# Performance work log

Measured on AMD Instinct MI355X. Metric: run time of the kernel, lower is better.

The kernel has to match this reference:

```python
import jax, jax.numpy as jnp
import numpy as np
from jax import lax

BS, C, H, W = 256, 256, 16, 16
NUM_CLASSES = 2
EPS = 1e-12  # F.normalize eps


def _l2_normalize(x):
    # F.normalize(x, dim=1, p=2): x / max(||x||_2, eps) along channel dim
    n = jnp.sqrt(jnp.sum(x * x, axis=1, keepdims=True))
    return x / jnp.maximum(n, EPS)


def _correlation(f1, f2):
    # original: (f1[:, :, None, :, :] * f2.reshape(bs,c,-1)[:, :, :, None, None]).sum(1)
    # -> [bs, h*w, h, w]; expressed as a batched contraction over channels.
    f1n = _l2_normalize(f1)                      # [bs, c, h, w]
    f2n = _l2_normalize(f2).reshape(f2.shape[0], f2.shape[1], -1)  # [bs, c, hw]
    return jnp.einsum('bcxy,bck->bkxy', f1n, f2n)


def _conv3x3(x, w, b):
    y = lax.conv_general_dilated(x, w, (1, 1), 'SAME',
                                 dimension_numbers=('NCHW', 'OIHW', 'NCHW'))
    return y + b[None, :, None, None]


def _psroi_diag(feat, num_classes, h, w):
    # full-image box, pooled==spatial, group_size==h -> each bin is one pixel:
    # out[n, c, ph, pw] = feat[n, (c*h + ph)*w + pw, ph, pw]
    bs = feat.shape[0]
    f = feat.reshape(bs, num_classes, h, w, h, w)
    f = jnp.diagonal(f, axis1=2, axis2=4)   # [bs, nc, w, w, h] (ph diag -> last)
    f = jnp.diagonal(f, axis1=2, axis2=3)   # [bs, nc, h, w]? -> [bs, nc, h_diag, w_diag]
    # after two diagonals axes are [bs, nc, ph, pw]
    return f


def setup_inputs() -> dict:
    key = jax.random.key(0)
    ks = jax.random.split(key, 5)
    std1 = float(np.sqrt(2.0 / (3 * 3 * 1024)))
    std2 = float(np.sqrt(2.0 / (3 * 3 * 512)))
    stdc = float(np.sqrt(2.0 / (1 * 1 * NUM_CLASSES * H * W)))
    return {
        'feature_1': jax.random.normal(ks[0], (BS, C, H, W), jnp.float32),
        'feature_2': jax.random.normal(ks[1], (BS, C, H, W), jnp.float32),
        'conv1_w': jax.random.normal(ks[2], (1024, 2 * (C + H * W), 3, 3), jnp.float32) * std1,
        'conv1_b': jnp.zeros((1024,), jnp.float32),
        'conv2_w': jax.random.normal(ks[3], (512, 1024, 3, 3), jnp.float32) * std2,
        'conv2_b': jnp.zeros((512,), jnp.float32),
        'conv_cls_w': jax.random.normal(ks[4], (NUM_CLASSES * H * W, 512, 1, 1), jnp.float32) * stdc,
    }


def reference(feature_1, feature_2, conv1_w, conv1_b, conv2_w, conv2_b, conv_cls_w):
    f1 = jax.nn.relu(feature_1)
    f2 = jax.nn.relu(feature_2)
    corr1 = _correlation(f1, f2)   # [bs, hw, h, w]
    corr2 = _correlation(f2, f1)
    feat = jnp.concatenate((f1, corr1, f2, corr2), axis=1)  # [bs, 2*(c+hw), h, w]
    feat = jax.nn.relu(_conv3x3(feat, conv1_w, conv1_b))
    feat = jax.nn.relu(_conv3x3(feat, conv2_w, conv2_b))
    feat = jnp.einsum('bchw,oc->bohw', feat, conv_cls_w[:, :, 0, 0])  # 1x1 conv, no bias
    feat = jax.nn.relu(feat)
    cls_base = _psroi_diag(feat, NUM_CLASSES, H, W)      # [bs, nc, h, w]
    cls_score = jnp.mean(cls_base, axis=(2, 3))          # AvgPool2d(h, w)
    cls_prob = jax.nn.softmax(cls_score, axis=1)
    # eval-mode return of the original module
    return (cls_prob, corr1, corr2)
```

## Files before the change

kernel.cpp:

```cpp
#include <hip/hip_runtime.h>


typedef __attribute__((ext_vector_type(8))) __bf16 bf16x8;
typedef __attribute__((ext_vector_type(4))) float f32x4;
typedef unsigned short u16;

template <bool B> struct BC { static constexpr bool value = B; };

__device__ __forceinline__ u16 f2bf(float f) {
  union { float f; unsigned u; } v; v.f = f;
  unsigned u = v.u;
  u += 0x7fffu + ((u >> 16) & 1u);
  return (u16)(u >> 16);
}
__device__ __forceinline__ float bf2f(u16 h) {
  union { unsigned u; float f; } v; v.u = ((unsigned)h) << 16;
  return v.f;
}
__device__ __forceinline__ void gl2lds16(const void* g, void* l) {
  __builtin_amdgcn_global_load_lds(
      (__attribute__((address_space(1))) void*)(void*)g,
      (__attribute__((address_space(3))) void*)l, 16, 0, 0);
}

__global__ __launch_bounds__(256) void k_norm(const float* __restrict__ f1,
                                              const float* __restrict__ f2,
                                              u16* __restrict__ featT,
                                              float* __restrict__ s1,
                                              float* __restrict__ s2) {
  int bx = blockIdx.x;
  int b = bx >> 2;
  int p0 = (bx & 3) << 6;
  int t = threadIdx.x;
  int p = p0 + (t & 63);
  int cg = t >> 6;
  int sp3 = ((p >> 1) & 3) << 3;
  const float* F1 = f1 + ((size_t)b << 16);
  const float* F2 = f2 + ((size_t)b << 16);
  u16* FT = featT + (((size_t)(b << 8) + p) << 10);
  float ss1 = 0.f, ss2 = 0.f;
  for (int i = 0; i < 64; ++i) {
    int c = (cg << 6) + i;
    float v1 = F1[(c << 8) + p]; v1 = v1 > 0.f ? v1 : 0.f;
    float v2 = F2[(c << 8) + p]; v2 = v2 > 0.f ? v2 : 0.f;
    ss1 += v1 * v1; ss2 += v2 * v2;
    FT[c ^ sp3] = f2bf(v1);
    FT[512 + (c ^ sp3)] = f2bf(v2);
  }
  __shared__ float l1[256], l2[256];
  l1[t] = ss1; l2[t] = ss2;
  __syncthreads();
  if (t < 64) {
    float a = l1[t] + l1[t + 64] + l1[t + 128] + l1[t + 192];
    float c2 = l2[t] + l2[t + 64] + l2[t + 128] + l2[t + 192];
    int pp = (b << 8) + p0 + t;
    s1[pp] = 1.f / fmaxf(sqrtf(a), 1e-12f);
    s2[pp] = 1.f / fmaxf(sqrtf(c2), 1e-12f);
  }
}

__global__ __launch_bounds__(256) void k_wconv(const float* __restrict__ w,
                                               u16* __restrict__ wb, int O, int C) {
  int o = blockIdx.x;
  int t = threadIdx.x;
  int sp3 = ((o >> 1) & 3) << 3;
  const float* src = w + (size_t)o * C * 9;
  for (int c = t; c < C; c += 256) {
    const float* s = src + c * 9;
    float v[9];
#pragma unroll
    for (int i = 0; i < 9; ++i) v[i] = s[i];
#pragma unroll
    for (int tap = 0; tap < 9; ++tap)
      wb[(size_t)tap * O * C + (size_t)o * C + (c ^ sp3)] = f2bf(v[tap]);
  }
}

__global__ __launch_bounds__(256) void k_corr(u16* featT,
                                              const float* __restrict__ s1,
                                              const float* __restrict__ s2,
                                              float* __restrict__ out) {
  __shared__ alignas(16) u16 Alds[128 * 32];
  __shared__ alignas(16) u16 Blds[128 * 32];
  __shared__ float tb[4][16][66];
  int bx = blockIdx.x;
  int b = bx >> 2;
  int p1b = ((bx >> 1) & 1) << 7;
  int p2b = (bx & 1) << 7;
  int t = threadIdx.x, l = t & 63, w = t >> 6;
  int wm = w >> 1, wn = w & 1, lr = l & 15, lq = l >> 4;
  int srow = (w << 4) + (l >> 2);
  int sq = (l & 3) << 3;
  int rsz = ((lq ^ ((lr >> 1) & 3)) << 3);
  const size_t bbase = (size_t)b << 18;

  f32x4 acc[4][4];
#pragma unroll
  for (int i = 0; i < 4; ++i)
#pragma unroll
    for (int j = 0; j < 4; ++j) acc[i][j] = (f32x4){0.f, 0.f, 0.f, 0.f};

#pragma unroll 1
  for (int kc = 0; kc < 8; ++kc) {
    int c0 = kc << 5;
    const u16* sA = featT + bbase + ((size_t)(p1b + srow) << 10) + (c0 + sq);
    gl2lds16(sA, Alds + ((w << 4) << 5));
    gl2lds16(sA + (64 << 10), Alds + ((64 + (w << 4)) << 5));
    const u16* sB = featT + bbase + ((size_t)(p2b + srow) << 10) + (512 + c0 + sq);
    gl2lds16(sB, Blds + ((w << 4) << 5));
    gl2lds16(sB + (64 << 10), Blds + ((64 + (w << 4)) << 5));
    __syncthreads();
    bf16x8 af[4], bfr[4];
#pragma unroll
    for (int mf = 0; mf < 4; ++mf)
      af[mf] = *(const bf16x8*)(Alds + (((wm << 6) + (mf << 4) + lr) << 5) + rsz);
#pragma unroll
    for (int nf = 0; nf < 4; ++nf)
      bfr[nf] = *(const bf16x8*)(Blds + (((wn << 6) + (nf << 4) + lr) << 5) + rsz);
#pragma unroll
    for (int mf = 0; mf < 4; ++mf)
#pragma unroll
      for (int nf = 0; nf < 4; ++nf)
        acc[mf][nf] = __builtin_amdgcn_mfma_f32_16x16x32_bf16(af[mf], bfr[nf], acc[mf][nf], 0, 0, 0);
    __syncthreads();
  }

  float sc2[4]; int p2g[4];
#pragma unroll
  for (int nf = 0; nf < 4; ++nf) {
    int p2 = p2b + (wn << 6) + (nf << 4) + lr;
    p2g[nf] = p2;
    sc2[nf] = s2[(b << 8) + p2];
  }
  float* corr1 = out + 512;
  float* corr2 = out + 512 + 16777216;
#pragma unroll
  for (int mf = 0; mf < 4; ++mf) {
    float gv[4][4];
#pragma unroll
    for (int r = 0; r < 4; ++r) {
      int p1 = p1b + (wm << 6) + (mf << 4) + (lq << 2) + r;
      float s1v = s1[(b << 8) + p1];
#pragma unroll
      for (int nf = 0; nf < 4; ++nf) gv[nf][r] = acc[mf][nf][r] * s1v * sc2[nf];
    }
#pragma unroll
    for (int r = 0; r < 4; ++r) {
      int p1 = p1b + (wm << 6) + (mf << 4) + (lq << 2) + r;
      int s1p3 = ((p1 >> 1) & 3) << 3;
#pragma unroll
      for (int nf = 0; nf < 4; ++nf) {
        corr2[((size_t)b << 16) + ((size_t)p1 << 8) + p2g[nf]] = gv[nf][r];
        featT[bbase + ((size_t)p1 << 10) + 256 + (p2g[nf] ^ s1p3)] = f2bf(gv[nf][r]);
      }
    }
#pragma unroll
    for (int r = 0; r < 4; ++r)
#pragma unroll
      for (int nf = 0; nf < 4; ++nf)
        tb[w][(lq << 2) + r][(nf << 4) + lr] = gv[nf][r];
#pragma unroll
    for (int j = 0; j < 16; ++j) {
      float v = tb[w][lr][(j << 2) + lq];
      int p2 = p2b + (wn << 6) + (j << 2) + lq;
      int s2p3 = ((p2 >> 1) & 3) << 3;
      int p1 = p1b + (wm << 6) + (mf << 4) + lr;
      corr1[((size_t)b << 16) + ((size_t)p2 << 8) + p1] = v;
      featT[bbase + ((size_t)p2 << 10) + 768 + (p1 ^ s2p3)] = f2bf(v);
    }
  }
}

template <int O, int OTB>
__global__ __launch_bounds__(512, 4) void k_conv(const u16* __restrict__ X,
                                                 const u16* __restrict__ Wb,
                                                 const float* __restrict__ bias,
                                                 u16* __restrict__ Out) {
  __shared__ alignas(16) u16 Xlds[2][260 * 32];
  __shared__ alignas(16) u16 Wlds[3][128 * 32];
  int bx = blockIdx.x;
  int otile = bx & ((1 << OTB) - 1);
  int b = bx >> OTB;
  int t = threadIdx.x, l = t & 63, w = t >> 6;
  int wm = w & 3, wn = w >> 2;
  int lr = l & 15, lq = l >> 4;
  int o0 = otile << 7;
  int srl = l >> 2;
  int sq = (l & 3) << 3;
  const size_t xbase = (size_t)b << 18;

  const u16* wsrc = Wb + (((size_t)(o0 + (w << 4) + srl)) << 10) + sq;
  const u16* xsrc0 = X + xbase + (((size_t)((w << 4) + srl)) << 10) + sq;
  const u16* xsrc1 = xsrc0 + ((size_t)128 << 10);

  u16* wdst0 = &Wlds[0][(w << 4) << 5];
  u16* wdst1 = &Wlds[1][(w << 4) << 5];
  u16* wdst2 = &Wlds[2][(w << 4) << 5];
  u16* xdA0 = &Xlds[0][(w << 4) << 5];
  u16* xdA1 = &Xlds[0][(128 + (w << 4)) << 5];
  u16* xdB0 = &Xlds[1][(w << 4) << 5];
  u16* xdB1 = &Xlds[1][(128 + (w << 4)) << 5];

  int rszw = ((lq ^ ((lr >> 1) & 3)) << 3);
  const u16* bwb0 = &Wlds[0][(((wn << 6) + lr) << 5) + rszw];
  const u16* bwb1 = &Wlds[1][(((wn << 6) + lr) << 5) + rszw];
  const u16* bwb2 = &Wlds[2][(((wn << 6) + lr) << 5) + rszw];

  int pb[4];
#pragma unroll
  for (int mf = 0; mf < 4; ++mf)
    pb[mf] = (((wm << 6) + (mf << 4) + lr) << 5);
  int xsz[3];
#pragma unroll
  for (int d = 0; d < 3; ++d)
    xsz[d] = ((lq ^ (((lr + d - 1) >> 1) & 3)) << 3);
  const int zoff = (256 << 5) + (lq << 3);

  f32x4 acc[4][4];
#pragma unroll
  for (int i = 0; i < 4; ++i)
#pragma unroll
    for (int j = 0; j < 4; ++j) acc[i][j] = (f32x4){0.f, 0.f, 0.f, 0.f};

  if (t < 32) ((unsigned*)&Xlds[t >> 4][256 << 5])[t & 15] = 0u;

  gl2lds16(xsrc0, xdA0);
  gl2lds16(xsrc1, xdA1);
  gl2lds16(wsrc, wdst0);
  gl2lds16(wsrc + ((size_t)O << 10), wdst1);
  __syncthreads();

  auto kcbody = [&](auto oddc, int kc) {
    constexpr bool ODD = decltype(oddc)::value;
    const u16* xb = ODD ? &Xlds[1][0] : &Xlds[0][0];
#pragma unroll
    for (int tap = 0; tap < 9; ++tap) {
      __builtin_amdgcn_sched_barrier(0);
      int ntap = (tap + 2) % 9;
      int nkc = kc + (tap >= 7 ? 1 : 0);
      u16* wd = ((tap + 2) % 3 == 0) ? wdst0 : (((tap + 2) % 3 == 1) ? wdst1 : wdst2);
      gl2lds16(wsrc + (size_t)ntap * ((size_t)O << 10) + (nkc << 5), wd);
      if (tap == 0) {
        if (ODD) { gl2lds16(xsrc0 + ((kc + 1) << 5), xdA0); gl2lds16(xsrc1 + ((kc + 1) << 5), xdA1); }
        else     { gl2lds16(xsrc0 + ((kc + 1) << 5), xdB0); gl2lds16(xsrc1 + ((kc + 1) << 5), xdB1); }
      }
      const u16* bwb = (tap % 3 == 0) ? bwb0 : ((tap % 3 == 1) ? bwb1 : bwb2);
      bf16x8 bwf[4];
#pragma unroll
      for (int nf = 0; nf < 4; ++nf) bwf[nf] = *(const bf16x8*)(bwb + (nf << 9));
      const int dr = tap / 3 - 1, dc = tap % 3 - 1;
      const int dpo = (((dr << 4) + dc) << 5) + xsz[dc + 1];
      bf16x8 axf[4];
#pragma unroll
      for (int mf = 0; mf < 4; ++mf) {
        int rr = (wm << 2) + mf + dr;
        bool v = ((unsigned)rr < 16u) & ((unsigned)(lr + dc) < 16u);
        int off = v ? (pb[mf] + dpo) : zoff;
        axf[mf] = *(const bf16x8*)(xb + off);
      }
#pragma unroll
      for (int mf = 0; mf < 4; ++mf)
#pragma unroll
        for (int nf = 0; nf < 4; ++nf)
          acc[mf][nf] = __builtin_amdgcn_mfma_f32_16x16x32_bf16(axf[mf], bwf[nf], acc[mf][nf], 0, 0, 0);
      if (tap == 0 || tap == 1) asm volatile("s_waitcnt vmcnt(3)" ::: "memory");
      else                      asm volatile("s_waitcnt vmcnt(1)" ::: "memory");
      __builtin_amdgcn_s_barrier();
    }
  };

#pragma unroll 1
  for (int kc2 = 0; kc2 < 16; ++kc2) {
    kcbody(BC<false>{}, 2 * kc2);
    kcbody(BC<true>{}, 2 * kc2 + 1);
  }

  __syncthreads();
  float bv[4];
#pragma unroll
  for (int nf = 0; nf < 4; ++nf) bv[nf] = bias[o0 + (wn << 6) + (nf << 4) + lr];
  u16* scr = ((u16*)Xlds) + w * 1152;
  int rr2 = l >> 2;
  int kq = l & 3;
#pragma unroll
  for (int mf = 0; mf < 4; ++mf) {
#pragma unroll
    for (int r = 0; r < 4; ++r) {
      int rr = (lq << 2) + r;
#pragma unroll
      for (int nf = 0; nf < 4; ++nf) {
        float vv = acc[mf][nf][r] + bv[nf];
        scr[rr * 72 + (nf << 4) + lr] = f2bf(vv > 0.f ? vv : 0.f);
      }
    }
    asm volatile("s_waitcnt lgkmcnt(0)" ::: "memory");
    __builtin_amdgcn_sched_barrier(0);
    int p = (wm << 6) + (mf << 4) + rr2;
    int sp = (p >> 1) & 3;
    size_t rbase = (size_t)((b << 8) + p) * O + (size_t)(o0 + (wn << 6));
#pragma unroll
    for (int j = 0; j < 2; ++j) {
      int k = (j << 2) | kq;
      int kl = (j << 2) | (kq ^ sp);
      uint4 v = *(const uint4*)(scr + rr2 * 72 + (kl << 3));
      *(uint4*)(Out + rbase + (k << 3)) = v;
    }
    asm volatile("s_waitcnt lgkmcnt(0)" ::: "memory");
    __builtin_amdgcn_sched_barrier(0);
  }
}

__global__ __launch_bounds__(256) void k_cls(const u16* __restrict__ X2,
                                             const float* __restrict__ Wc,
                                             float* __restrict__ out) {
  int b = blockIdx.x, p = threadIdx.x;
  int s = (p >> 1) & 3;
  const uint4* xv = (const uint4*)(X2 + (((size_t)(b << 8) + p) << 9));
  const float4* w0 = (const float4*)(Wc + ((size_t)p << 9));
  const float4* w1 = (const float4*)(Wc + ((size_t)(256 + p) << 9));
  float a0 = 0.f, a1 = 0.f;
#pragma unroll 4
  for (int i = 0; i < 64; ++i) {
    int ii = (i & ~3) | ((i & 3) ^ s);
    uint4 u = xv[ii];
    float x0 = bf2f((u16)(u.x & 0xffffu)), x1 = bf2f((u16)(u.x >> 16));
    float x2 = bf2f((u16)(u.y & 0xffffu)), x3 = bf2f((u16)(u.y >> 16));
    float x4 = bf2f((u16)(u.z & 0xffffu)), x5 = bf2f((u16)(u.z >> 16));
    float x6 = bf2f((u16)(u.w & 0xffffu)), x7 = bf2f((u16)(u.w >> 16));
    float4 wa = w0[i * 2], wb = w0[i * 2 + 1];
    a0 += x0 * wa.x + x1 * wa.y + x2 * wa.z + x3 * wa.w +
          x4 * wb.x + x5 * wb.y + x6 * wb.z + x7 * wb.w;
    float4 wc4 = w1[i * 2], wd = w1[i * 2 + 1];
    a1 += x0 * wc4.x + x1 * wc4.y + x2 * wc4.z + x3 * wc4.w +
          x4 * wd.x + x5 * wd.y + x6 * wd.z + x7 * wd.w;
  }
  a0 = fmaxf(a0, 0.f);
  a1 = fmaxf(a1, 0.f);
  __shared__ float r0[256], r1[256];
  r0[p] = a0; r1[p] = a1;
  for (int sdx = 128; sdx > 0; sdx >>= 1) {
    __syncthreads();
    if (p < sdx) { r0[p] += r0[p + sdx]; r1[p] += r1[p + sdx]; }
  }
  __syncthreads();
  if (p == 0) {
    float s0 = r0[0] * (1.f / 256.f), s1v = r1[0] * (1.f / 256.f);
    float m = fmaxf(s0, s1v);
    float e0 = expf(s0 - m), e1 = expf(s1v - m);
    float inv = 1.f / (e0 + e1);
    out[(b << 1) + 0] = e0 * inv;
    out[(b << 1) + 1] = e1 * inv;
  }
}

extern "C" void kernel_launch(void* const* d_in, const int* in_sizes, int n_in,
                              void* d_out, int out_size, void* d_ws, size_t ws_size,
                              hipStream_t stream) {
  const float* f1 = (const float*)d_in[0];
  const float* f2 = (const float*)d_in[1];
  const float* w1 = (const float*)d_in[2];
  const float* b1 = (const float*)d_in[3];
  const float* w2 = (const float*)d_in[4];
  const float* b2 = (const float*)d_in[5];
  const float* wc = (const float*)d_in[6];
  float* out = (float*)d_out;
  char* ws = (char*)d_ws;

  u16* featT = (u16*)(ws + 0);
  u16* out1T = (u16*)(ws + 134217728);
  u16* W1b   = (u16*)(ws + 268435456);
  u16* W2b   = (u16*)(ws + 287309824);
  float* s1  = (float*)(ws + 296747008);
  float* s2  = (float*)(ws + 297009152);
  u16* out2T = (u16*)(ws + 0);

  k_norm<<<1024, 256, 0, stream>>>(f1, f2, featT, s1, s2);
  k_wconv<<<1024, 256, 0, stream>>>(w1, W1b, 1024, 1024);
  k_wconv<<<512, 256, 0, stream>>>(w2, W2b, 512, 1024);
  k_corr<<<1024, 256, 0, stream>>>(featT, s1, s2, out);
  k_conv<1024, 3><<<2048, 512, 0, stream>>>(featT, W1b, b1, out1T);
  k_conv<512, 2><<<1024, 512, 0, stream>>>(out1T, W2b, b2, out2T);
  k_cls<<<256, 256, 0, stream>>>(out2T, wc, out);
}
```

Measured before the change: 1.902 ms.

## Deepen conv weight prefetch to four LDS buffers and raise MFMA priority

The conv kernel's weight staging grows from three to four rotating LDS buffers, so weight tiles are prefetched three taps ahead instead of two. The k-chunk loop is unrolled by four to keep the buffer rotation compile-time, and the vmcnt waits are relaxed to match. s_setprio is raised around the MFMA block so compute waves are favoured over load issue. The cls kernel now reads the X2 rows in linear order and applies the swizzle to the weight index instead; this uses more LDS per block and enlarges code size, which may affect occupancy.

```diff
diff --git a/kernel.cpp b/kernel.cpp
--- a/kernel.cpp
+++ b/kernel.cpp
@@ -5,7 +5,7 @@
 typedef __attribute__((ext_vector_type(4))) float f32x4;
 typedef unsigned short u16;
 
-template <bool B> struct BC { static constexpr bool value = B; };
+template <int I> struct IC { static constexpr int value = I; };
 
 __device__ __forceinline__ u16 f2bf(float f) {
   union { float f; unsigned u; } v; v.f = f;
@@ -177,7 +177,7 @@
                                                  const float* __restrict__ bias,
                                                  u16* __restrict__ Out) {
   __shared__ alignas(16) u16 Xlds[2][260 * 32];
-  __shared__ alignas(16) u16 Wlds[3][128 * 32];
+  __shared__ alignas(16) u16 Wlds[4][128 * 32];
   int bx = blockIdx.x;
   int otile = bx & ((1 << OTB) - 1);
   int b = bx >> OTB;
@@ -196,6 +196,7 @@
   u16* wdst0 = &Wlds[0][(w << 4) << 5];
   u16* wdst1 = &Wlds[1][(w << 4) << 5];
   u16* wdst2 = &Wlds[2][(w << 4) << 5];
+  u16* wdst3 = &Wlds[3][(w << 4) << 5];
   u16* xdA0 = &Xlds[0][(w << 4) << 5];
   u16* xdA1 = &Xlds[0][(128 + (w << 4)) << 5];
   u16* xdB0 = &Xlds[1][(w << 4) << 5];
@@ -205,6 +206,7 @@
   const u16* bwb0 = &Wlds[0][(((wn << 6) + lr) << 5) + rszw];
   const u16* bwb1 = &Wlds[1][(((wn << 6) + lr) << 5) + rszw];
   const u16* bwb2 = &Wlds[2][(((wn << 6) + lr) << 5) + rszw];
+  const u16* bwb3 = &Wlds[3][(((wn << 6) + lr) << 5) + rszw];
 
   int pb[4];
 #pragma unroll
@@ -228,23 +230,32 @@
   gl2lds16(xsrc1, xdA1);
   gl2lds16(wsrc, wdst0);
   gl2lds16(wsrc + ((size_t)O << 10), wdst1);
-  __syncthreads();
-
-  auto kcbody = [&](auto oddc, int kc) {
-    constexpr bool ODD = decltype(oddc)::value;
-    const u16* xb = ODD ? &Xlds[1][0] : &Xlds[0][0];
+  gl2lds16(wsrc + 2 * ((size_t)O << 10), wdst2);
+  asm volatile("s_waitcnt vmcnt(2) lgkmcnt(0)" ::: "memory");
+  __builtin_amdgcn_s_barrier();
+
+  auto kcbody = [&](auto km4c, int kc) {
+    constexpr int KM4 = decltype(km4c)::value;
+    const u16* xb = (KM4 & 1) ? &Xlds[1][0] : &Xlds[0][0];
 #pragma unroll
     for (int tap = 0; tap < 9; ++tap) {
       __builtin_amdgcn_sched_barrier(0);
-      int ntap = (tap + 2) % 9;
-      int nkc = kc + (tap >= 7 ? 1 : 0);
-      u16* wd = ((tap + 2) % 3 == 0) ? wdst0 : (((tap + 2) % 3 == 1) ? wdst1 : wdst2);
-      gl2lds16(wsrc + (size_t)ntap * ((size_t)O << 10) + (nkc << 5), wd);
+      {
+        int ntap = (tap + 3 > 8) ? (tap - 6) : (tap + 3);
+        int nkc = (tap >= 6) ? (kc + 1) : kc;
+        constexpr int WB = (KM4 + 3) & 3;
+        u16* wd = (((WB + tap) & 3) == 0) ? wdst0
+                : ((((WB + tap) & 3) == 1) ? wdst1
+                : ((((WB + tap) & 3) == 2) ? wdst2 : wdst3));
+        gl2lds16(wsrc + (size_t)ntap * ((size_t)O << 10) + (nkc << 5), wd);
+      }
       if (tap == 0) {
-        if (ODD) { gl2lds16(xsrc0 + ((kc + 1) << 5), xdA0); gl2lds16(xsrc1 + ((kc + 1) << 5), xdA1); }
-        else     { gl2lds16(xsrc0 + ((kc + 1) << 5), xdB0); gl2lds16(xsrc1 + ((kc + 1) << 5), xdB1); }
-      }
-      const u16* bwb = (tap % 3 == 0) ? bwb0 : ((tap % 3 == 1) ? bwb1 : bwb2);
+        if (KM4 & 1) { gl2lds16(xsrc0 + ((kc + 1) << 5), xdA0); gl2lds16(xsrc1 + ((kc + 1) << 5), xdA1); }
+        else         { gl2lds16(xsrc0 + ((kc + 1) << 5), xdB0); gl2lds16(xsrc1 + ((kc + 1) << 5), xdB1); }
+      }
+      const u16* bwb = (((KM4 + tap) & 3) == 0) ? bwb0
+                     : ((((KM4 + tap) & 3) == 1) ? bwb1
+                     : ((((KM4 + tap) & 3) == 2) ? bwb2 : bwb3));
       bf16x8 bwf[4];
 #pragma unroll
       for (int nf = 0; nf < 4; ++nf) bwf[nf] = *(const bf16x8*)(bwb + (nf << 9));
@@ -258,21 +269,25 @@
         int off = v ? (pb[mf] + dpo) : zoff;
         axf[mf] = *(const bf16x8*)(xb + off);
       }
+      __builtin_amdgcn_s_setprio(1);
 #pragma unroll
       for (int mf = 0; mf < 4; ++mf)
 #pragma unroll
         for (int nf = 0; nf < 4; ++nf)
           acc[mf][nf] = __builtin_amdgcn_mfma_f32_16x16x32_bf16(axf[mf], bwf[nf], acc[mf][nf], 0, 0, 0);
-      if (tap == 0 || tap == 1) asm volatile("s_waitcnt vmcnt(3)" ::: "memory");
-      else                      asm volatile("s_waitcnt vmcnt(1)" ::: "memory");
+      __builtin_amdgcn_s_setprio(0);
+      if (tap <= 2) asm volatile("s_waitcnt vmcnt(4)" ::: "memory");
+      else          asm volatile("s_waitcnt vmcnt(2)" ::: "memory");
       __builtin_amdgcn_s_barrier();
     }
   };
 
 #pragma unroll 1
-  for (int kc2 = 0; kc2 < 16; ++kc2) {
-    kcbody(BC<false>{}, 2 * kc2);
-    kcbody(BC<true>{}, 2 * kc2 + 1);
+  for (int kc4 = 0; kc4 < 8; ++kc4) {
+    kcbody(IC<0>{}, 4 * kc4);
+    kcbody(IC<1>{}, 4 * kc4 + 1);
+    kcbody(IC<2>{}, 4 * kc4 + 2);
+    kcbody(IC<3>{}, 4 * kc4 + 3);
   }
 
   __syncthreads();
@@ -321,16 +336,16 @@
   float a0 = 0.f, a1 = 0.f;
 #pragma unroll 4
   for (int i = 0; i < 64; ++i) {
-    int ii = (i & ~3) | ((i & 3) ^ s);
-    uint4 u = xv[ii];
+    uint4 u = xv[i];
+    int il = (i & ~3) | ((i & 3) ^ s);
     float x0 = bf2f((u16)(u.x & 0xffffu)), x1 = bf2f((u16)(u.x >> 16));
     float x2 = bf2f((u16)(u.y & 0xffffu)), x3 = bf2f((u16)(u.y >> 16));
     float x4 = bf2f((u16)(u.z & 0xffffu)), x5 = bf2f((u16)(u.z >> 16));
     float x6 = bf2f((u16)(u.w & 0xffffu)), x7 = bf2f((u16)(u.w >> 16));
-    float4 wa = w0[i * 2], wb = w0[i * 2 + 1];
+    float4 wa = w0[il * 2], wb = w0[il * 2 + 1];
     a0 += x0 * wa.x + x1 * wa.y + x2 * wa.z + x3 * wa.w +
           x4 * wb.x + x5 * wb.y + x6 * wb.z + x7 * wb.w;
-    float4 wc4 = w1[i * 2], wd = w1[i * 2 + 1];
+    float4 wc4 = w1[il * 2], wd = w1[il * 2 + 1];
     a1 += x0 * wc4.x + x1 * wc4.y + x2 * wc4.z + x3 * wc4.w +
           x4 * wd.x + x5 * wd.y + x6 * wd.z + x7 * wd.w;
   }
```

Measured after the change: 2.250 ms. 18.3% more time.
